# Kernel tuning notes

Hardware: AMD Instinct MI355X
Metric: run time of the kernel (lower is better)

The kernel has to match this reference:

```python
import jax, jax.numpy as jnp
import numpy as np

N = 100000       # nodes
E = 1600000      # edges (avg degree 16)
D_IN = 64
D_H = 64
D_OUT = 32
G = 64           # graphs in the batch


def setup_inputs() -> dict:
    key = jax.random.key(0)
    ks = jax.random.split(key, 10)
    x = jnp.zeros((N,), dtype=jnp.int32)  # embedding vocab is 1 -> all indices 0
    edge_index = jax.random.randint(ks[0], (2, E), 0, N, dtype=jnp.int32)
    batch = jnp.sort(jax.random.randint(ks[1], (N,), 0, G, dtype=jnp.int32))
    emb = jax.random.normal(ks[2], (1, D_IN), dtype=jnp.float32)
    W1 = jax.random.normal(ks[3], (D_IN, D_H), dtype=jnp.float32) * 0.05
    b1 = jax.random.normal(ks[4], (D_H,), dtype=jnp.float32) * 0.05
    W2 = jax.random.normal(ks[5], (D_H, D_H), dtype=jnp.float32) * 0.05
    b2 = jax.random.normal(ks[6], (D_H,), dtype=jnp.float32) * 0.05
    fcW = jax.random.normal(ks[7], (D_H, D_OUT), dtype=jnp.float32) * 0.05
    fcb = jax.random.normal(ks[8], (D_OUT,), dtype=jnp.float32) * 0.05
    return {"x": x, "edge_index": edge_index, "batch": batch, "emb": emb,
            "W1": W1, "b1": b1, "W2": W2, "b2": b2, "fcW": fcW, "fcb": fcb}


def _gcn_conv(h, W, b, src, dst):
    # PyG GCNConv with add_self_loops=True, symmetric normalization:
    # out = D^{-1/2} (A + I) D^{-1/2} (h @ W) + b, with deg computed on dst + self loop.
    h = h @ W  # [N, D]
    deg = jnp.zeros((N,), h.dtype).at[dst].add(1.0) + 1.0  # +1 for self loop
    dinv = jax.lax.rsqrt(deg)  # [N]
    norm = dinv[src] * dinv[dst]  # [E]
    agg = jax.ops.segment_sum(h[src] * norm[:, None], dst, num_segments=N)
    # self-loop term: norm_ii = dinv_i * dinv_i
    return agg + h * (dinv * dinv)[:, None] + b


def reference(x, edge_index, batch, emb, W1, b1, W2, b2, fcW, fcb):
    src, dst = edge_index[0], edge_index[1]
    h = emb[x]  # [N, D_IN] embedding lookup
    h = jax.nn.relu(_gcn_conv(h, W1, b1, src, dst))
    # dropout is identity in eval mode
    h = jax.nn.relu(_gcn_conv(h, W2, b2, src, dst))
    # global mean pool per graph
    sums = jax.ops.segment_sum(h, batch, num_segments=G)            # [G, D_H]
    cnt = jax.ops.segment_sum(jnp.ones((N,), h.dtype), batch, num_segments=G)
    pooled = sums / jnp.maximum(cnt, 1.0)[:, None]
    return pooled @ fcW + fcb  # [G, D_OUT]
```

## Files before the change

kernel.cpp:

```cpp
#include <hip/hip_runtime.h>
#include <hip/hip_bf16.h>


#define DH 64
#define DOUT 32
#define NBIN 65
#define BW 64
#define MAXNB 2048
#define SCAN_N 2048
#define SRCM 0x3FFFFFF
#define CAPE 1280
#define GPB 256
#define NSH 8

__global__ __launch_bounds__(1024) void k_group(
        const int* __restrict__ src, const int* __restrict__ dst,
        unsigned* __restrict__ rec, unsigned short* __restrict__ idx,
        const float* __restrict__ emb, const float* __restrict__ W1,
        const float* __restrict__ b1, const float* __restrict__ W2,
        float* __restrict__ tarr, float2* __restrict__ PQ, int E, int NB, int chunk) {
    __shared__ int lh[SCAN_N];
    __shared__ int lb[SCAN_N];
    __shared__ float ewl[DH], tl[DH], bl[DH];
    __shared__ int rl[DH], sl[DH];
    int tid = threadIdx.x, bid = blockIdx.x;
    if (bid >= GPB) {
        int beta = bid - GPB;
        int k = tid;
        float s = 0.f, t = 0.f;
        if (k < DH) {
#pragma unroll
            for (int j = 0; j < DH; ++j) s += emb[j] * W1[j * DH + k];
            t = (s != 0.f) ? (-b1[k] / s) : INFINITY;
            ewl[k] = s; tl[k] = t; bl[k] = b1[k];
        }
        __syncthreads();
        if (k < DH) {
            int r = 0, ss = 0;
#pragma unroll
            for (int j = 0; j < DH; ++j) { r += (tl[j] <= t); ss += (tl[j] < t); }
            rl[k] = r; sl[k] = ss;
            if (beta == 0) tarr[k] = t;
        }
        __syncthreads();
        if (k < DH) {
            float p = 0.f, q = 0.f;
            for (int kk = 0; kk < DH; ++kk) {
                float e = ewl[kk];
                bool act;
                if (e > 0.f) act = (beta >= rl[kk]);
                else if (e < 0.f) act = (beta <= sl[kk]);
                else act = (bl[kk] > 0.f);
                if (act) {
                    float w = W2[kk * DH + k];
                    p += e * w;
                    q += bl[kk] * w;
                }
            }
            PQ[beta * DH + k] = make_float2(p, q);
        }
        return;
    }
    int c0 = bid * chunk;
    int c1 = min(c0 + chunk, E);
    for (int t = tid; t < SCAN_N; t += 1024) lh[t] = 0;
    __syncthreads();
    for (int e = c0 + tid; e < c1; e += 1024)
        atomicAdd(&lh[dst[e] >> 6], 1);
    __syncthreads();
    for (int t = tid; t < SCAN_N; t += 1024) lb[t] = lh[t];
    __syncthreads();
    for (int ofs = 1; ofs < SCAN_N; ofs <<= 1) {
        int i1 = tid + 1024;
        int v0 = (tid >= ofs) ? lb[tid - ofs] : 0;
        int v1 = (i1 >= ofs) ? lb[i1 - ofs] : 0;
        __syncthreads();
        lb[tid] += v0; lb[i1] += v1;
        __syncthreads();
    }
    size_t ib = (size_t)bid * (MAXNB + 1);
    for (int t = tid; t < NB; t += 1024) {
        int base = lb[t] - lh[t];
        idx[ib + t] = (unsigned short)base;
        lb[t] = base;
    }
    if (tid == 0) idx[ib + NB] = (unsigned short)(c1 - c0);
    __syncthreads();
    for (int t = tid; t < NB; t += 1024) lh[t] = 0;
    __syncthreads();
    for (int e = c0 + tid; e < c1; e += 1024) {
        int s = src[e], dd = dst[e];
        int bk = dd >> 6;
        int o = lb[bk] + atomicAdd(&lh[bk], 1);
        rec[(size_t)bid * chunk + o] = (unsigned)s | ((unsigned)(dd & 63) << 26);
    }
}

__global__ __launch_bounds__(256) void k_passA(const unsigned short* __restrict__ idx,
        const unsigned* __restrict__ rec, unsigned* __restrict__ rec2,
        int* __restrict__ cnts, float* __restrict__ dinv, int N, int chunk) {
    __shared__ int rst[GPB];
    __shared__ int ps[GPB];
    __shared__ int cl[BW];
    int tid = threadIdx.x, bk = blockIdx.x;
    if (tid < BW) cl[tid] = 0;
    if (tid < GPB) {
        size_t ib = (size_t)tid * (MAXNB + 1);
        int s = idx[ib + bk];
        int e = idx[ib + bk + 1];
        rst[tid] = tid * chunk + s;
        ps[tid] = e - s;
    }
    __syncthreads();
    for (int ofs = 1; ofs < GPB; ofs <<= 1) {
        int v = (tid < GPB && tid >= ofs) ? ps[tid - ofs] : 0;
        __syncthreads();
        if (tid < GPB) ps[tid] += v;
        __syncthreads();
    }
    int T = ps[GPB - 1];
    if (tid == 0) cnts[bk] = min(T, CAPE);
    size_t r2 = (size_t)bk * CAPE;
    for (int o = tid; o < T; o += 256) {
        int r = 0;
#pragma unroll
        for (int s = 128; s > 0; s >>= 1)
            if (r + s <= GPB && ps[r + s - 1] <= o) r += s;
        int base = (r > 0) ? ps[r - 1] : 0;
        unsigned v = rec[rst[r] + (o - base)];
        atomicAdd(&cl[v >> 26], 1);
        if (o < CAPE) rec2[r2 + o] = v;
    }
    __syncthreads();
    if (tid < BW) {
        int i = bk * BW + tid;
        if (i < N) dinv[i] = rsqrtf((float)cl[tid] + 1.0f);
    }
}

__global__ __launch_bounds__(256, 8) void k_passB(const int* __restrict__ cnts,
        const unsigned* __restrict__ rec2, const float* __restrict__ dinv,
        const float* __restrict__ tarr, float4* __restrict__ summary,
        int* __restrict__ flags, int N) {
    __shared__ float Sl[BW];
    __shared__ float tl[DH];
    int tid = threadIdx.x;
    if (tid < BW) Sl[tid] = 0.f;
    if (tid < DH) tl[tid] = tarr[tid];
    __syncthreads();
    int b = blockIdx.x;
    int cnt = cnts[b];
    size_t r0 = (size_t)b * CAPE;
    const uint4* rq = (const uint4*)(rec2 + r0);
    int nq = cnt >> 2;
    for (int q = tid; q < nq; q += blockDim.x) {
        uint4 r = rq[q];
        float d0 = dinv[r.x & SRCM];
        float d1 = dinv[r.y & SRCM];
        float d2 = dinv[r.z & SRCM];
        float d3 = dinv[r.w & SRCM];
        atomicAdd(&Sl[r.x >> 26], d0);
        atomicAdd(&Sl[r.y >> 26], d1);
        atomicAdd(&Sl[r.z >> 26], d2);
        atomicAdd(&Sl[r.w >> 26], d3);
    }
    int e = (nq << 2) + tid;
    if (e < cnt) {
        unsigned r = rec2[r0 + e];
        atomicAdd(&Sl[r >> 26], dinv[r & SRCM]);
    }
    __syncthreads();
    if (tid < BW) {
        int i = b * BW + tid;
        if (i < N) {
            float di = dinv[i];
            float c = di * (Sl[tid] + di);
            int bb = 0;
#pragma unroll
            for (int j = 0; j < DH; ++j) bb += (tl[j] < c);
            summary[i] = make_float4(di * c, di, __uint_as_float((unsigned)bb), 0.f);
            flags[bb] = 1;
        }
    }
}

__global__ __launch_bounds__(256, 4) void k_passC(const int* __restrict__ cnts,
        const unsigned* __restrict__ rec2, const float4* __restrict__ summary,
        const float2* __restrict__ PQ, const int* __restrict__ flags,
        const float* __restrict__ b2, const int* __restrict__ batch,
        float* __restrict__ psum_s, float* __restrict__ cnt_s, int N, int G) {
    __shared__ __align__(16) float AB[BW * NBIN * 2];
    __shared__ unsigned char ulist[NBIN + 3];
    __shared__ int UcntS;
    int tid = threadIdx.x;
    if (tid < 64) {
        int act = (flags[tid] != 0);
        unsigned long long m = __ballot(act);
        int pos = __popcll(m & ((1ull << tid) - 1ull));
        if (act) ulist[pos] = (unsigned char)tid;
        if (tid == 0) {
            int total = __popcll(m);
            if (flags[64]) ulist[total++] = 64;
            UcntS = total;
        }
    }
    float4* AB4 = (float4*)AB;
    for (int t = tid; t < (BW * NBIN * 2) / 4; t += blockDim.x)
        AB4[t] = make_float4(0.f, 0.f, 0.f, 0.f);
    __syncthreads();
    int b = blockIdx.x;
    int ecnt = cnts[b];
    size_t r0 = (size_t)b * CAPE;
    const uint4* rq = (const uint4*)(rec2 + r0);
    int nq = ecnt >> 2;
    for (int q = tid; q < nq; q += blockDim.x) {
        uint4 r = rq[q];
        float4 s0 = summary[r.x & SRCM];
        float4 s1 = summary[r.y & SRCM];
        float4 s2 = summary[r.z & SRCM];
        float4 s3 = summary[r.w & SRCM];
        float* p0 = &AB[(((r.x >> 26)) * NBIN + __float_as_uint(s0.z)) * 2];
        atomicAdd(p0, s0.x); atomicAdd(p0 + 1, s0.y);
        float* p1 = &AB[(((r.y >> 26)) * NBIN + __float_as_uint(s1.z)) * 2];
        atomicAdd(p1, s1.x); atomicAdd(p1 + 1, s1.y);
        float* p2 = &AB[(((r.z >> 26)) * NBIN + __float_as_uint(s2.z)) * 2];
        atomicAdd(p2, s2.x); atomicAdd(p2 + 1, s2.y);
        float* p3 = &AB[(((r.w >> 26)) * NBIN + __float_as_uint(s3.z)) * 2];
        atomicAdd(p3, s3.x); atomicAdd(p3 + 1, s3.y);
    }
    int e = (nq << 2) + tid;
    if (e < ecnt) {
        unsigned r = rec2[r0 + e];
        float4 sm = summary[r & SRCM];
        float* pp = &AB[((r >> 26) * NBIN + __float_as_uint(sm.z)) * 2];
        atomicAdd(pp, sm.x); atomicAdd(pp + 1, sm.y);
    }
    __syncthreads();
    int U = UcntS;
    int d = tid & 63;
    int w = tid >> 6;
    int n0b = w << 4;
    float2 abr[16];
#pragma unroll
    for (int j = 0; j < 16; ++j)
        abr[j] = *(const float2*)&AB[((n0b + j) * NBIN + d) * 2];
    float accv[16];
#pragma unroll
    for (int j = 0; j < 16; ++j) accv[j] = 0.f;
    for (int uu = 0; uu < U; ++uu) {
        int u = ulist[uu];
        float2 pq = PQ[u * DH + d];
        if (u < 64) {
#pragma unroll
            for (int j = 0; j < 16; ++j) {
                float ax = __int_as_float(__builtin_amdgcn_readlane(__float_as_int(abr[j].x), u));
                float ay = __int_as_float(__builtin_amdgcn_readlane(__float_as_int(abr[j].y), u));
                accv[j] += ax * pq.x + ay * pq.y;
            }
        } else {
#pragma unroll
            for (int j = 0; j < 16; ++j) {
                float2 v = *(const float2*)&AB[((n0b + j) * NBIN + 64) * 2];
                accv[j] += v.x * pq.x + v.y * pq.y;
            }
        }
    }
    float* psum = psum_s + (size_t)(b & (NSH - 1)) * G * DH;
    float* cnt  = cnt_s  + (size_t)(b & (NSH - 1)) * G;
    int n0 = b * BW;
    float bias = b2[d];
    float lsum = 0.f, lcnt = 0.f;
    int cb = -1;
    for (int j = 0; j < 16; ++j) {
        int i = n0 + n0b + j;
        if (i >= N) break;
        float4 sm = summary[i];
        int rb = (int)__float_as_uint(sm.z);
        float2 pq = PQ[rb * DH + d];
        float g = sm.x * pq.x + sm.y * pq.y;
        float v = fmaxf(sm.y * (accv[j] + g) + bias, 0.f);
        int bt = batch[i];
        if (bt != cb) {
            if (cb >= 0) {
                atomicAdd(&psum[cb * DH + d], lsum);
                if (d == 0) atomicAdd(&cnt[cb], lcnt);
            }
            cb = bt; lsum = 0.f; lcnt = 0.f;
        }
        lsum += v;
        if (d == 0) lcnt += 1.f;
    }
    if (cb >= 0) {
        atomicAdd(&psum[cb * DH + d], lsum);
        if (d == 0) atomicAdd(&cnt[cb], lcnt);
    }
}

__global__ __launch_bounds__(64) void k_out(const float* __restrict__ psum_s,
        const float* __restrict__ cnt_s, const float* __restrict__ fcW,
        const float* __restrict__ fcb, float* __restrict__ out, int G) {
    __shared__ float pooled[DH];
    int g = blockIdx.x, d = threadIdx.x;
    float s = 0.f, cc = 0.f;
#pragma unroll
    for (int k = 0; k < NSH; ++k) {
        s += psum_s[(size_t)k * G * DH + g * DH + d];
        cc += cnt_s[(size_t)k * G + g];
    }
    pooled[d] = s / fmaxf(cc, 1.0f);
    __syncthreads();
    if (d < DOUT) {
        float o = 0.f;
#pragma unroll
        for (int kk = 0; kk < DH; ++kk) o += pooled[kk] * fcW[kk * DOUT + d];
        out[g * DOUT + d] = o + fcb[d];
    }
}

static inline size_t pad256(size_t n) { return (n + 255) & ~(size_t)255; }

extern "C" void kernel_launch(void* const* d_in, const int* in_sizes, int n_in,
                              void* d_out, int out_size, void* d_ws, size_t ws_size,
                              hipStream_t stream) {
    const int N = in_sizes[0];
    const int E = in_sizes[1] / 2;
    const int G = out_size / DOUT;
    const int NB = (N + BW - 1) / BW;
    const int chunk = (E + GPB - 1) / GPB;

    const int* edge = (const int*)d_in[1];
    const int* src = edge;
    const int* dst = edge + E;
    const int* batch = (const int*)d_in[2];
    const float* emb = (const float*)d_in[3];
    const float* W1 = (const float*)d_in[4];
    const float* b1 = (const float*)d_in[5];
    const float* W2 = (const float*)d_in[6];
    const float* b2 = (const float*)d_in[7];
    const float* fcW = (const float*)d_in[8];
    const float* fcb = (const float*)d_in[9];
    float* out = (float*)d_out;

    char* ws = (char*)d_ws;
    size_t off = 0;
    float* psum_s = (float*)(ws + off); off += pad256((size_t)NSH * G * DH) * 4;
    float* cnt_s  = (float*)(ws + off); off += pad256((size_t)NSH * G) * 4;
    int* flags  = (int*)(ws + off);    off += pad256(NBIN) * 4;
    size_t zero_bytes = off;
    unsigned* rec  = (unsigned*)(ws + off); off += pad256((size_t)GPB * chunk) * 4;
    unsigned* rec2 = (unsigned*)(ws + off); off += pad256((size_t)MAXNB * CAPE) * 4;
    unsigned short* idx = (unsigned short*)(ws + off);
    off += pad256((size_t)GPB * (MAXNB + 1)) * 2;
    int* cnts    = (int*)(ws + off);    off += pad256(MAXNB) * 4;
    float* dinv  = (float*)(ws + off);  off += pad256(N) * 4;
    float* tarr  = (float*)(ws + off);  off += pad256(DH) * 4;
    float2* PQ   = (float2*)(ws + off); off += pad256(NBIN * DH) * 8;
    float4* summary = (float4*)(ws + off); off += pad256(N) * 16;

    hipMemsetAsync(d_ws, 0, zero_bytes, stream);

    const int B = 256;
    k_group<<<GPB + NBIN, 1024, 0, stream>>>(src, dst, rec, idx, emb, W1, b1, W2,
                                             tarr, PQ, E, NB, chunk);
    k_passA<<<NB, B, 0, stream>>>(idx, rec, rec2, cnts, dinv, N, chunk);
    k_passB<<<NB, B, 0, stream>>>(cnts, rec2, dinv, tarr, summary, flags, N);
    k_passC<<<NB, B, 0, stream>>>(cnts, rec2, summary, PQ, flags, b2, batch,
                                  psum_s, cnt_s, N, G);
    k_out<<<G, 64, 0, stream>>>(psum_s, cnt_s, fcW, fcb, out, G);
}
```

Before: 163.8 us.

## Split edge grouping into more, smaller blocks with per-thread serial prefix scan

The grouping kernel now runs 512 blocks of 256 threads instead of 256 blocks of 1024 threads, so each block handles a smaller chunk of edges. The 2048-bin shared-memory scan is replaced by a per-thread serial scan over 8 bins followed by a 256-wide block scan, and the zeroing of histogram bins is folded into the same loop. passA is adapted to gather and scan 512 per-block segments per bucket, which adds work to its binary search and scan. The aim is better occupancy and fewer barriers in k_group, paid for with more segments to merge downstream.

```diff
diff --git a/kernel.cpp b/kernel.cpp
--- a/kernel.cpp
+++ b/kernel.cpp
@@ -10,10 +10,11 @@
 #define SCAN_N 2048
 #define SRCM 0x3FFFFFF
 #define CAPE 1280
-#define GPB 256
+#define GPB 512
+#define GT 256
 #define NSH 8
 
-__global__ __launch_bounds__(1024) void k_group(
+__global__ __launch_bounds__(256) void k_group(
         const int* __restrict__ src, const int* __restrict__ dst,
         unsigned* __restrict__ rec, unsigned short* __restrict__ idx,
         const float* __restrict__ emb, const float* __restrict__ W1,
@@ -21,6 +22,7 @@
         float* __restrict__ tarr, float2* __restrict__ PQ, int E, int NB, int chunk) {
     __shared__ int lh[SCAN_N];
     __shared__ int lb[SCAN_N];
+    __shared__ int wt[GT];
     __shared__ float ewl[DH], tl[DH], bl[DH];
     __shared__ int rl[DH], sl[DH];
     int tid = threadIdx.x, bid = blockIdx.x;
@@ -63,32 +65,38 @@
     }
     int c0 = bid * chunk;
     int c1 = min(c0 + chunk, E);
-    for (int t = tid; t < SCAN_N; t += 1024) lh[t] = 0;
-    __syncthreads();
-    for (int e = c0 + tid; e < c1; e += 1024)
+    for (int t = tid; t < SCAN_N; t += GT) lh[t] = 0;
+    __syncthreads();
+    for (int e = c0 + tid; e < c1; e += GT)
         atomicAdd(&lh[dst[e] >> 6], 1);
     __syncthreads();
-    for (int t = tid; t < SCAN_N; t += 1024) lb[t] = lh[t];
-    __syncthreads();
-    for (int ofs = 1; ofs < SCAN_N; ofs <<= 1) {
-        int i1 = tid + 1024;
-        int v0 = (tid >= ofs) ? lb[tid - ofs] : 0;
-        int v1 = (i1 >= ofs) ? lb[i1 - ofs] : 0;
-        __syncthreads();
-        lb[tid] += v0; lb[i1] += v1;
-        __syncthreads();
-    }
+    int base8 = tid << 3;
+    int l[8], pfx[8];
+#pragma unroll
+    for (int k = 0; k < 8; ++k) l[k] = lh[base8 + k];
+    int tot = 0;
+#pragma unroll
+    for (int k = 0; k < 8; ++k) { pfx[k] = tot; tot += l[k]; }
+    wt[tid] = tot;
+    __syncthreads();
+    for (int ofs = 1; ofs < GT; ofs <<= 1) {
+        int v = (tid >= ofs) ? wt[tid - ofs] : 0;
+        __syncthreads();
+        wt[tid] += v;
+        __syncthreads();
+    }
+    int excl = wt[tid] - tot;
     size_t ib = (size_t)bid * (MAXNB + 1);
-    for (int t = tid; t < NB; t += 1024) {
-        int base = lb[t] - lh[t];
-        idx[ib + t] = (unsigned short)base;
-        lb[t] = base;
+#pragma unroll
+    for (int k = 0; k < 8; ++k) {
+        int v = excl + pfx[k];
+        lb[base8 + k] = v;
+        if (base8 + k < NB) idx[ib + base8 + k] = (unsigned short)v;
+        lh[base8 + k] = 0;
     }
     if (tid == 0) idx[ib + NB] = (unsigned short)(c1 - c0);
     __syncthreads();
-    for (int t = tid; t < NB; t += 1024) lh[t] = 0;
-    __syncthreads();
-    for (int e = c0 + tid; e < c1; e += 1024) {
+    for (int e = c0 + tid; e < c1; e += GT) {
         int s = src[e], dd = dst[e];
         int bk = dd >> 6;
         int o = lb[bk] + atomicAdd(&lh[bk], 1);
@@ -104,18 +112,20 @@
     __shared__ int cl[BW];
     int tid = threadIdx.x, bk = blockIdx.x;
     if (tid < BW) cl[tid] = 0;
-    if (tid < GPB) {
-        size_t ib = (size_t)tid * (MAXNB + 1);
+    for (int t = tid; t < GPB; t += 256) {
+        size_t ib = (size_t)t * (MAXNB + 1);
         int s = idx[ib + bk];
         int e = idx[ib + bk + 1];
-        rst[tid] = tid * chunk + s;
-        ps[tid] = e - s;
+        rst[t] = t * chunk + s;
+        ps[t] = e - s;
     }
     __syncthreads();
     for (int ofs = 1; ofs < GPB; ofs <<= 1) {
-        int v = (tid < GPB && tid >= ofs) ? ps[tid - ofs] : 0;
-        __syncthreads();
-        if (tid < GPB) ps[tid] += v;
+        int i0 = tid, i1 = tid + 256;
+        int v0 = (i0 >= ofs) ? ps[i0 - ofs] : 0;
+        int v1 = (i1 >= ofs) ? ps[i1 - ofs] : 0;
+        __syncthreads();
+        ps[i0] += v0; ps[i1] += v1;
         __syncthreads();
     }
     int T = ps[GPB - 1];
@@ -124,7 +134,7 @@
     for (int o = tid; o < T; o += 256) {
         int r = 0;
 #pragma unroll
-        for (int s = 128; s > 0; s >>= 1)
+        for (int s = 256; s > 0; s >>= 1)
             if (r + s <= GPB && ps[r + s - 1] <= o) r += s;
         int base = (r > 0) ? ps[r - 1] : 0;
         unsigned v = rec[rst[r] + (o - base)];
@@ -326,7 +336,8 @@
     const int E = in_sizes[1] / 2;
     const int G = out_size / DOUT;
     const int NB = (N + BW - 1) / BW;
-    const int chunk = (E + GPB - 1) / GPB;
+    int chunk = (E + GPB - 1) / GPB;
+    chunk = (chunk + 3) & ~3;
 
     const int* edge = (const int*)d_in[1];
     const int* src = edge;
@@ -360,8 +371,8 @@
     hipMemsetAsync(d_ws, 0, zero_bytes, stream);
 
     const int B = 256;
-    k_group<<<GPB + NBIN, 1024, 0, stream>>>(src, dst, rec, idx, emb, W1, b1, W2,
-                                             tarr, PQ, E, NB, chunk);
+    k_group<<<GPB + NBIN, GT, 0, stream>>>(src, dst, rec, idx, emb, W1, b1, W2,
+                                           tarr, PQ, E, NB, chunk);
     k_passA<<<NB, B, 0, stream>>>(idx, rec, rec2, cnts, dinv, N, chunk);
     k_passB<<<NB, B, 0, stream>>>(cnts, rec2, dinv, tarr, summary, flags, N);
     k_passC<<<NB, B, 0, stream>>>(cnts, rec2, summary, PQ, flags, b2, batch,
```

New measurement: 165.8 us. About the same (+1.2%).
